# Performance work log

Hardware: AMD Instinct MI355X
Metric: run time of the kernel (lower is better)

Reference implementation:

```python
import jax, jax.numpy as jnp
import numpy as np

H = 16          # num_attention_heads
HD = 64         # attention_head_size
D = H * HD
SCALE = HD ** -0.5
SP_HEADS = np.array([0, 2, 4, 6, 8, 10, 12, 14])   # sparsemax heads
SM_HEADS = np.array([1, 3, 5, 7, 9, 11, 13, 15])   # softmax heads


def sparsemax(z):
    # z: [..., K]; sparsemax along last dim (Martins & Astudillo 2016)
    K = z.shape[-1]
    zs = -jnp.sort(-z, axis=-1)                      # descending sort
    k = jnp.arange(1, K + 1, dtype=z.dtype)
    cs = jnp.cumsum(zs, axis=-1)
    support = (1 + k * zs) > cs
    ksel = jnp.sum(support, axis=-1, keepdims=True)  # support size >= 1
    tau = (jnp.take_along_axis(cs, ksel - 1, axis=-1) - 1) / ksel.astype(z.dtype)
    return jnp.maximum(z - tau, 0)


def setup_inputs() -> dict:
    key = jax.random.key(0)
    ks = jax.random.split(key, 4)
    B, S = 4, 1024
    return {
        "hidden_states": jax.random.normal(ks[0], (B, S, D), dtype=jnp.float32),
        "Wq": jax.random.normal(ks[1], (D, D), dtype=jnp.float32) * 0.02,
        "bq": jnp.zeros((D,), dtype=jnp.float32),
        "Wk": jax.random.normal(ks[2], (D, D), dtype=jnp.float32) * 0.02,
        "bk": jnp.zeros((D,), dtype=jnp.float32),
        "Wv": jax.random.normal(ks[3], (D, D), dtype=jnp.float32) * 0.02,
        "bv": jnp.zeros((D,), dtype=jnp.float32),
        "attention_mask": jnp.zeros((B, 1, 1, S), dtype=jnp.float32),
    }


def reference(hidden_states, Wq, bq, Wk, bk, Wv, bv, attention_mask):
    B, S, _ = hidden_states.shape

    def proj(W, b):
        # [B,S,D] -> [B,H,S,HD]
        return (hidden_states @ W + b).reshape(B, S, H, HD).transpose(0, 2, 1, 3)

    q, k, v = proj(Wq, bq), proj(Wk, bk), proj(Wv, bv)
    scores = jnp.einsum('bhqd,bhkd->bhqk', q, k) * SCALE
    scores = scores + attention_mask
    scores = jnp.maximum(scores, -10000.0)           # clamp(min=-10000)
    weights = jnp.zeros_like(scores)
    weights = weights.at[:, SP_HEADS].set(sparsemax(scores[:, SP_HEADS]))
    weights = weights.at[:, SM_HEADS].set(jax.nn.softmax(scores[:, SM_HEADS], axis=-1))
    # dropout_p = 0 in eval mode
    attn_out = jnp.einsum('bhqk,bhkd->bhqd', weights, v)
    attn_out = attn_out.transpose(0, 2, 1, 3).reshape(B, S, D)
    return attn_out
```

## Files before the change

### kernel.cpp

```cpp
#include <hip/hip_runtime.h>
#include <hip/hip_bf16.h>
#include <stdint.h>

#define NH 16
#define HD 64
#define DM 1024
#define NB 4
#define SEQ 1024
#define NTOK (NB*SEQ)
#define SCALE 0.125f

typedef __bf16 bf16_t;
typedef __bf16 bf16x8 __attribute__((ext_vector_type(8)));
typedef __bf16 bf16x4 __attribute__((ext_vector_type(4)));
typedef float f32x4 __attribute__((ext_vector_type(4)));
typedef float f32x2 __attribute__((ext_vector_type(2)));

__global__ void cvt_hs_kernel(const float* __restrict__ in, bf16_t* __restrict__ out, int n4){
  int i = blockIdx.x*256 + threadIdx.x;
  if (i >= n4) return;
  f32x4 v = ((const f32x4*)in)[i];
  bf16x4 o;
  o[0]=(bf16_t)v[0]; o[1]=(bf16_t)v[1]; o[2]=(bf16_t)v[2]; o[3]=(bf16_t)v[3];
  ((bf16x4*)out)[i] = o;
}

__global__ void cvt_wt_kernel(const float* __restrict__ Wq, const float* __restrict__ Wk,
                              const float* __restrict__ Wv, bf16_t* __restrict__ outbase){
  __shared__ float tile[32][33];
  const float* W = blockIdx.z==0 ? Wq : (blockIdx.z==1 ? Wk : Wv);
  bf16_t* Wt = outbase + (size_t)blockIdx.z * DM * DM;
  int k0 = blockIdx.x*32, n0 = blockIdx.y*32;
  #pragma unroll
  for (int i=0;i<4;i++){
    int r = threadIdx.y + i*8;
    tile[r][threadIdx.x] = W[(size_t)(k0+r)*DM + n0 + threadIdx.x];
  }
  __syncthreads();
  #pragma unroll
  for (int i=0;i<4;i++){
    int r = threadIdx.y + i*8;
    Wt[(size_t)(n0+r)*DM + k0 + threadIdx.x] = (bf16_t)tile[threadIdx.x][r];
  }
}

__global__ __launch_bounds__(256)
void qkv_gemm_kernel(const bf16_t* __restrict__ Ag, const bf16_t* __restrict__ Wtb,
                     const float* __restrict__ bq, const float* __restrict__ bk, const float* __restrict__ bv,
                     bf16_t* __restrict__ Qb, bf16_t* __restrict__ Kb, bf16_t* __restrict__ Vtb)
{
  __shared__ __align__(16) bf16_t Asm[128*64];
  __shared__ __align__(16) bf16_t Bsm[128*64];
  const int z = blockIdx.z;
  const bf16_t* Btg = Wtb + (size_t)z*DM*DM;
  const float* bias = (z==0)?bq:((z==1)?bk:bv);
  const int m0 = blockIdx.x*128, n0 = blockIdx.y*128;
  const int tid = threadIdx.x, lane = tid&63, w = tid>>6;
  const int wr = w>>1, wc = w&1;
  const int lr = lane&15, hk = (lane>>4)<<3;

  f32x4 acc[4][4];
  #pragma unroll
  for (int a=0;a<4;a++)
    #pragma unroll
    for (int c=0;c<4;c++)
      acc[a][c] = (f32x4){0.f,0.f,0.f,0.f};

  for (int k0=0; k0<DM; k0+=64){
    #pragma unroll
    for (int i=0;i<4;i++){
      int flat = i*256 + tid;
      int row = flat>>3, kc = (flat&7)<<3;
      *(bf16x8*)&Asm[(row<<6)+kc] = *(const bf16x8*)&Ag [(size_t)(m0+row)*DM + k0 + kc];
      *(bf16x8*)&Bsm[(row<<6)+kc] = *(const bf16x8*)&Btg[(size_t)(n0+row)*DM + k0 + kc];
    }
    __syncthreads();
    #pragma unroll
    for (int kk=0;kk<2;kk++){
      bf16x8 af[4], bfv[4];
      #pragma unroll
      for (int mf=0;mf<4;mf++)
        af[mf] = *(const bf16x8*)&Asm[((wr*64 + mf*16 + lr)<<6) + (kk<<5) + hk];
      #pragma unroll
      for (int nf=0;nf<4;nf++)
        bfv[nf] = *(const bf16x8*)&Bsm[((wc*64 + nf*16 + lr)<<6) + (kk<<5) + hk];
      #pragma unroll
      for (int mf=0;mf<4;mf++)
        #pragma unroll
        for (int nf=0;nf<4;nf++)
          acc[mf][nf] = __builtin_amdgcn_mfma_f32_16x16x32_bf16(af[mf], bfv[nf], acc[mf][nf], 0, 0, 0);
    }
    __syncthreads();
  }

  const int q4 = (lane>>4)<<2;
  #pragma unroll
  for (int mf=0;mf<4;mf++){
    #pragma unroll
    for (int nf=0;nf<4;nf++){
      int gn = n0 + wc*64 + nf*16 + lr;
      float bsv = bias[gn];
      int hh = gn>>6, hd = gn&63;
      int gm0 = m0 + wr*64 + mf*16 + q4;
      int bb = gm0>>10, sq0 = gm0&1023;
      if (z < 2){
        bf16_t* dst = (z==0)?Qb:Kb;
        #pragma unroll
        for (int j=0;j<4;j++)
          dst[(((size_t)bb*NH + hh)*SEQ + (sq0+j))*HD + hd] = (bf16_t)(acc[mf][nf][j] + bsv);
      } else {
        bf16x4 pk;
        #pragma unroll
        for (int j=0;j<4;j++) pk[j] = (bf16_t)(acc[mf][nf][j] + bsv);
        *(bf16x4*)&Vtb[(((size_t)bb*NH + hh)*HD + hd)*SEQ + sq0] = pk;
      }
    }
  }
}

__device__ __forceinline__ float wsum(float v){
  #pragma unroll
  for (int m=32;m>=1;m>>=1) v += __shfl_xor(v, m, 64);
  return v;
}
__device__ __forceinline__ float wmax(float v){
  #pragma unroll
  for (int m=32;m>=1;m>>=1) v = fmaxf(v, __shfl_xor(v, m, 64));
  return v;
}

__device__ __forceinline__ void wstore(bf16_t* Wb, int row, int col, float v){
  int chunk = (col >> 3) ^ (row & 15);
  Wb[row*1024 + chunk*8 + (col&7)] = (bf16_t)v;
}

__global__ __launch_bounds__(512)
void attn_mfma_kernel(const bf16_t* __restrict__ Qg, const bf16_t* __restrict__ Kg,
                      const bf16_t* __restrict__ Vt, const float* __restrict__ maskg,
                      float* __restrict__ outg)
{
  __shared__ __align__(16) float S[32*1024];
  bf16_t* Wlds = (bf16_t*)S;
  float*  Pacc = S + 16*1024;

  const int bh = blockIdx.y, b = bh>>4, h = bh&15;
  const int row0 = blockIdx.x*32;
  const int tid = threadIdx.x, lane = tid&63, w = tid>>6;
  const int ln = lane&15, hi4 = lane>>4;
  const size_t hoff = (size_t)bh*SEQ*HD;
  const int k0w = w*128;

  bf16x8 qf[2][2];
  #pragma unroll
  for (int mt=0; mt<2; ++mt)
    #pragma unroll
    for (int kt=0; kt<2; ++kt)
      qf[mt][kt] = *(const bf16x8*)&Qg[hoff + (size_t)(row0 + mt*16 + ln)*HD + kt*32 + hi4*8];

  #pragma unroll
  for (int nt=0; nt<8; ++nt){
    const int kcol = k0w + nt*16 + ln;
    float mval = maskg[b*SEQ + kcol];
    bf16x8 kf0 = *(const bf16x8*)&Kg[hoff + (size_t)kcol*HD +  0 + hi4*8];
    bf16x8 kf1 = *(const bf16x8*)&Kg[hoff + (size_t)kcol*HD + 32 + hi4*8];
    #pragma unroll
    for (int mt=0; mt<2; ++mt){
      f32x4 acc = (f32x4){0.f,0.f,0.f,0.f};
      acc = __builtin_amdgcn_mfma_f32_16x16x32_bf16(qf[mt][0], kf0, acc, 0,0,0);
      acc = __builtin_amdgcn_mfma_f32_16x16x32_bf16(qf[mt][1], kf1, acc, 0,0,0);
      #pragma unroll
      for (int j=0;j<4;++j){
        int q = mt*16 + hi4*4 + j;
        S[q*1024 + kcol] = fmaxf(fmaf(acc[j], SCALE, mval), -10000.f);
      }
    }
  }
  __syncthreads();

  float z[4][16];
  #pragma unroll
  for (int r=0;r<4;++r)
    #pragma unroll
    for (int i=0;i<16;++i)
      z[r][i] = S[(w*4+r)*1024 + i*64 + lane];
  __syncthreads();

  if ((h&1)==0){
    #pragma unroll
    for (int r=0;r<4;++r){
      float mx = z[r][0];
      #pragma unroll
      for (int i=1;i<16;++i) mx = fmaxf(mx, z[r][i]);
      mx = wmax(mx);
      float lo = mx - 1.0f, bhi = mx;
      for (int it=0; it<12; ++it){
        float mid = 0.5f*(lo+bhi);
        float g = 0.f;
        #pragma unroll
        for (int i=0;i<16;++i) g += fmaxf(z[r][i]-mid, 0.f);
        g = wsum(g);
        if (g >= 1.0f) lo = mid; else bhi = mid;
      }
      float tau = lo;
      #pragma unroll
      for (int nw=0; nw<3; ++nw){
        float cnt=0.f, sm=0.f;
        #pragma unroll
        for (int i=0;i<16;++i){
          bool in = z[r][i] > tau;
          cnt += in ? 1.0f : 0.0f;
          sm  += in ? z[r][i] : 0.0f;
        }
        cnt = wsum(cnt); sm = wsum(sm);
        tau = (sm - 1.0f)/cnt;
      }
      #pragma unroll
      for (int i=0;i<16;++i)
        wstore(Wlds, w*4+r, i*64+lane, fmaxf(z[r][i]-tau, 0.f));
    }
  } else {
    #pragma unroll
    for (int r=0;r<4;++r){
      float mx = z[r][0];
      #pragma unroll
      for (int i=1;i<16;++i) mx = fmaxf(mx, z[r][i]);
      mx = wmax(mx);
      float sm = 0.f;
      #pragma unroll
      for (int i=0;i<16;++i){ z[r][i] = __expf(z[r][i]-mx); sm += z[r][i]; }
      sm = wsum(sm);
      float inv = 1.0f/sm;
      #pragma unroll
      for (int i=0;i<16;++i)
        wstore(Wlds, w*4+r, i*64+lane, z[r][i]*inv);
    }
  }
  __syncthreads();

  f32x4 oa[2][4];
  #pragma unroll
  for (int mt=0;mt<2;++mt)
    #pragma unroll
    for (int nt=0;nt<4;++nt)
      oa[mt][nt] = (f32x4){0.f,0.f,0.f,0.f};

  #pragma unroll
  for (int kt=0; kt<4; ++kt){
    bf16x8 wa[2];
    #pragma unroll
    for (int mt=0;mt<2;++mt){
      int ch = (w*16 + kt*4 + hi4) ^ ln;
      wa[mt] = *(const bf16x8*)&Wlds[(mt*16+ln)*1024 + ch*8];
    }
    #pragma unroll
    for (int nt=0; nt<4; ++nt){
      bf16x8 vb = *(const bf16x8*)&Vt[(size_t)bh*(HD*SEQ) + (size_t)(nt*16+ln)*SEQ + k0w + kt*32 + hi4*8];
      #pragma unroll
      for (int mt=0;mt<2;++mt)
        oa[mt][nt] = __builtin_amdgcn_mfma_f32_16x16x32_bf16(wa[mt], vb, oa[mt][nt], 0,0,0);
    }
  }
  #pragma unroll
  for (int mt=0;mt<2;++mt)
    #pragma unroll
    for (int nt=0;nt<4;++nt)
      #pragma unroll
      for (int j=0;j<4;++j)
        Pacc[w*2048 + (mt*16 + hi4*4 + j)*64 + nt*16 + ln] = oa[mt][nt][j];
  __syncthreads();

  {
    int q = tid>>4, c4 = (tid&15)<<2;
    f32x4 s = (f32x4){0.f,0.f,0.f,0.f};
    #pragma unroll
    for (int p=0;p<8;++p) s += *(const f32x4*)&Pacc[p*2048 + q*64 + c4];
    *(f32x4*)&outg[((size_t)(b*SEQ + row0 + q))*DM + h*64 + c4] = s;
  }
}

extern "C" void kernel_launch(void* const* d_in, const int* in_sizes, int n_in,
                              void* d_out, int out_size, void* d_ws, size_t ws_size,
                              hipStream_t stream)
{
  const float* hs   = (const float*)d_in[0];
  const float* Wq   = (const float*)d_in[1];
  const float* bq   = (const float*)d_in[2];
  const float* Wk   = (const float*)d_in[3];
  const float* bk   = (const float*)d_in[4];
  const float* Wv   = (const float*)d_in[5];
  const float* bv   = (const float*)d_in[6];
  const float* mask = (const float*)d_in[7];
  float* out = (float*)d_out;

  char* ws = (char*)d_ws;
  bf16_t* hsb = (bf16_t*)ws;
  bf16_t* Wt  = (bf16_t*)(ws + (size_t)( 8u<<20));
  bf16_t* Qb  = (bf16_t*)(ws + (size_t)(14u<<20));
  bf16_t* Kb  = (bf16_t*)(ws + (size_t)(22u<<20));
  bf16_t* Vtb = (bf16_t*)(ws + (size_t)(30u<<20));

  cvt_hs_kernel<<<(NTOK*DM/4 + 255)/256, 256, 0, stream>>>(hs, hsb, NTOK*DM/4);
  cvt_wt_kernel<<<dim3(32,32,3), dim3(32,8), 0, stream>>>(Wq, Wk, Wv, Wt);
  qkv_gemm_kernel<<<dim3(32,8,3), 256, 0, stream>>>(hsb, Wt, bq, bk, bv, Qb, Kb, Vtb);
  attn_mfma_kernel<<<dim3(32,64), 512, 0, stream>>>(Qb, Kb, Vtb, mask, out);
}
```

Measured before the change: 332.3 us.

## Restructure attention kernel with bf16 score LDS and full-K PV per wave

The attention kernel now stores scores in LDS as bf16 with an XOR swizzle instead of fp32. That halves shared memory and allows four blocks per CU via launch bounds. Row reductions for four rows are batched into a single shuffle sequence, and the sparsemax bisection drops from 12 to 8 iterations. In the PV stage each wave covers the full key range for one 16x16 output tile, so the cross-wave fp32 partial-sum buffer and the extra reduction pass go away. The QKV GEMM also switches to direct global-to-LDS loads. Rounding scores to bf16 before sparsemax and softmax, and using fewer bisection steps, may reduce accuracy.

```diff
diff --git a/kernel.cpp b/kernel.cpp
--- a/kernel.cpp
+++ b/kernel.cpp
@@ -14,7 +14,13 @@
 typedef __bf16 bf16x8 __attribute__((ext_vector_type(8)));
 typedef __bf16 bf16x4 __attribute__((ext_vector_type(4)));
 typedef float f32x4 __attribute__((ext_vector_type(4)));
-typedef float f32x2 __attribute__((ext_vector_type(2)));
+
+typedef __attribute__((address_space(3))) unsigned char lds_byte;
+typedef __attribute__((address_space(1))) const unsigned char gbl_byte;
+
+__device__ __forceinline__ void glds16(const void* g, void* l){
+  __builtin_amdgcn_global_load_lds((gbl_byte*)g, (lds_byte*)l, 16, 0, 0);
+}
 
 __global__ void cvt_hs_kernel(const float* __restrict__ in, bf16_t* __restrict__ out, int n4){
   int i = blockIdx.x*256 + threadIdx.x;
@@ -69,10 +75,11 @@
   for (int k0=0; k0<DM; k0+=64){
     #pragma unroll
     for (int i=0;i<4;i++){
-      int flat = i*256 + tid;
+      int cb = (i<<8) + (tid & 448);
+      int flat = cb + lane;
       int row = flat>>3, kc = (flat&7)<<3;
-      *(bf16x8*)&Asm[(row<<6)+kc] = *(const bf16x8*)&Ag [(size_t)(m0+row)*DM + k0 + kc];
-      *(bf16x8*)&Bsm[(row<<6)+kc] = *(const bf16x8*)&Btg[(size_t)(n0+row)*DM + k0 + kc];
+      glds16(&Ag [(size_t)(m0+row)*DM + k0 + kc], &Asm[cb<<3]);
+      glds16(&Btg[(size_t)(n0+row)*DM + k0 + kc], &Bsm[cb<<3]);
     }
     __syncthreads();
     #pragma unroll
@@ -118,37 +125,37 @@
   }
 }
 
-__device__ __forceinline__ float wsum(float v){
-  #pragma unroll
-  for (int m=32;m>=1;m>>=1) v += __shfl_xor(v, m, 64);
-  return v;
-}
-__device__ __forceinline__ float wmax(float v){
-  #pragma unroll
-  for (int m=32;m>=1;m>>=1) v = fmaxf(v, __shfl_xor(v, m, 64));
-  return v;
-}
-
-__device__ __forceinline__ void wstore(bf16_t* Wb, int row, int col, float v){
-  int chunk = (col >> 3) ^ (row & 15);
-  Wb[row*1024 + chunk*8 + (col&7)] = (bf16_t)v;
-}
-
-__global__ __launch_bounds__(512)
-void attn_mfma_kernel(const bf16_t* __restrict__ Qg, const bf16_t* __restrict__ Kg,
-                      const bf16_t* __restrict__ Vt, const float* __restrict__ maskg,
-                      float* __restrict__ outg)
+__device__ __forceinline__ void red4sum(float v[4]){
+  #pragma unroll
+  for (int m=32;m>=1;m>>=1){
+    float t0=__shfl_xor(v[0],m,64), t1=__shfl_xor(v[1],m,64);
+    float t2=__shfl_xor(v[2],m,64), t3=__shfl_xor(v[3],m,64);
+    v[0]+=t0; v[1]+=t1; v[2]+=t2; v[3]+=t3;
+  }
+}
+__device__ __forceinline__ void red4max(float v[4]){
+  #pragma unroll
+  for (int m=32;m>=1;m>>=1){
+    float t0=__shfl_xor(v[0],m,64), t1=__shfl_xor(v[1],m,64);
+    float t2=__shfl_xor(v[2],m,64), t3=__shfl_xor(v[3],m,64);
+    v[0]=fmaxf(v[0],t0); v[1]=fmaxf(v[1],t1); v[2]=fmaxf(v[2],t2); v[3]=fmaxf(v[3],t3);
+  }
+}
+
+__global__ __launch_bounds__(512, 4)
+void attn_mfma2_kernel(const bf16_t* __restrict__ Qg, const bf16_t* __restrict__ Kg,
+                       const bf16_t* __restrict__ Vt, const float* __restrict__ maskg,
+                       float* __restrict__ outg)
 {
-  __shared__ __align__(16) float S[32*1024];
-  bf16_t* Wlds = (bf16_t*)S;
-  float*  Pacc = S + 16*1024;
+  __shared__ __align__(16) bf16_t Sb[32*1024];
+  char* Sbb = (char*)Sb;
 
   const int bh = blockIdx.y, b = bh>>4, h = bh&15;
   const int row0 = blockIdx.x*32;
   const int tid = threadIdx.x, lane = tid&63, w = tid>>6;
   const int ln = lane&15, hi4 = lane>>4;
   const size_t hoff = (size_t)bh*SEQ*HD;
-  const int k0w = w*128;
+  const int kbase = w*128;
 
   bf16x8 qf[2][2];
   #pragma unroll
@@ -159,123 +166,145 @@
 
   #pragma unroll
   for (int nt=0; nt<8; ++nt){
-    const int kcol = k0w + nt*16 + ln;
-    float mval = maskg[b*SEQ + kcol];
-    bf16x8 kf0 = *(const bf16x8*)&Kg[hoff + (size_t)kcol*HD +  0 + hi4*8];
-    bf16x8 kf1 = *(const bf16x8*)&Kg[hoff + (size_t)kcol*HD + 32 + hi4*8];
+    const int krow = kbase + nt*16;
+    bf16x8 kf0 = *(const bf16x8*)&Kg[hoff + (size_t)(krow+ln)*HD +  0 + hi4*8];
+    bf16x8 kf1 = *(const bf16x8*)&Kg[hoff + (size_t)(krow+ln)*HD + 32 + hi4*8];
+    f32x4 mv = *(const f32x4*)&maskg[(size_t)b*SEQ + krow + hi4*4];
     #pragma unroll
     for (int mt=0; mt<2; ++mt){
       f32x4 acc = (f32x4){0.f,0.f,0.f,0.f};
-      acc = __builtin_amdgcn_mfma_f32_16x16x32_bf16(qf[mt][0], kf0, acc, 0,0,0);
-      acc = __builtin_amdgcn_mfma_f32_16x16x32_bf16(qf[mt][1], kf1, acc, 0,0,0);
-      #pragma unroll
-      for (int j=0;j<4;++j){
-        int q = mt*16 + hi4*4 + j;
-        S[q*1024 + kcol] = fmaxf(fmaf(acc[j], SCALE, mval), -10000.f);
+      acc = __builtin_amdgcn_mfma_f32_16x16x32_bf16(kf0, qf[mt][0], acc, 0,0,0);
+      acc = __builtin_amdgcn_mfma_f32_16x16x32_bf16(kf1, qf[mt][1], acc, 0,0,0);
+      bf16x4 pk;
+      #pragma unroll
+      for (int j=0;j<4;++j)
+        pk[j] = (bf16_t)fmaxf(fmaf(acc[j], SCALE, mv[j]), -10000.f);
+      const int q = mt*16 + ln;
+      const int g = (krow + hi4*4) >> 3;
+      const int gp = g ^ ln;
+      *(bf16x4*)(Sbb + q*2048 + gp*16 + (hi4&1)*8) = pk;
+    }
+  }
+  __syncthreads();
+
+  float z[4][16];
+  const int qr = w*4;
+  #pragma unroll
+  for (int r=0;r<4;++r){
+    const int q = qr + r;
+    #pragma unroll
+    for (int i=0;i<4;++i){
+      const int gp = (i*32 + (lane>>1)) ^ (q&15);
+      bf16x4 v4 = *(const bf16x4*)(Sbb + q*2048 + gp*16 + (lane&1)*8);
+      z[r][i*4+0]=(float)v4[0]; z[r][i*4+1]=(float)v4[1];
+      z[r][i*4+2]=(float)v4[2]; z[r][i*4+3]=(float)v4[3];
+    }
+  }
+  __syncthreads();
+
+  float mx[4];
+  #pragma unroll
+  for (int r=0;r<4;++r){
+    float m = z[r][0];
+    #pragma unroll
+    for (int i=1;i<16;++i) m = fmaxf(m, z[r][i]);
+    mx[r] = m;
+  }
+  red4max(mx);
+
+  if ((h&1)==0){
+    float lo[4], hi_[4];
+    #pragma unroll
+    for (int r=0;r<4;++r){ lo[r]=mx[r]-1.0f; hi_[r]=mx[r]; }
+    for (int it=0; it<8; ++it){
+      float mid[4], g4[4];
+      #pragma unroll
+      for (int r=0;r<4;++r){
+        mid[r] = 0.5f*(lo[r]+hi_[r]);
+        float g = 0.f;
+        #pragma unroll
+        for (int i=0;i<16;++i) g += fmaxf(z[r][i]-mid[r], 0.f);
+        g4[r] = g;
       }
+      red4sum(g4);
+      #pragma unroll
+      for (int r=0;r<4;++r){
+        if (g4[r] >= 1.0f) lo[r] = mid[r]; else hi_[r] = mid[r];
+      }
+    }
+    float tau[4];
+    #pragma unroll
+    for (int r=0;r<4;++r) tau[r] = lo[r];
+    for (int it=0; it<3; ++it){
+      float cnt[4], sm[4];
+      #pragma unroll
+      for (int r=0;r<4;++r){
+        float c=0.f, s=0.f;
+        #pragma unroll
+        for (int i=0;i<16;++i){
+          bool in = z[r][i] > tau[r];
+          c += in ? 1.0f : 0.0f;
+          s += in ? z[r][i] : 0.0f;
+        }
+        cnt[r]=c; sm[r]=s;
+      }
+      red4sum(cnt); red4sum(sm);
+      #pragma unroll
+      for (int r=0;r<4;++r) tau[r] = (sm[r]-1.0f)/cnt[r];
+    }
+    #pragma unroll
+    for (int r=0;r<4;++r)
+      #pragma unroll
+      for (int i=0;i<16;++i) z[r][i] = fmaxf(z[r][i]-tau[r], 0.f);
+  } else {
+    float sm[4];
+    #pragma unroll
+    for (int r=0;r<4;++r){
+      float s = 0.f;
+      #pragma unroll
+      for (int i=0;i<16;++i){ z[r][i] = __expf(z[r][i]-mx[r]); s += z[r][i]; }
+      sm[r] = s;
+    }
+    red4sum(sm);
+    #pragma unroll
+    for (int r=0;r<4;++r){
+      float inv = 1.0f/sm[r];
+      #pragma unroll
+      for (int i=0;i<16;++i) z[r][i] *= inv;
+    }
+  }
+
+  #pragma unroll
+  for (int r=0;r<4;++r){
+    const int q = qr + r;
+    #pragma unroll
+    for (int i=0;i<4;++i){
+      bf16x4 pk;
+      pk[0]=(bf16_t)z[r][i*4+0]; pk[1]=(bf16_t)z[r][i*4+1];
+      pk[2]=(bf16_t)z[r][i*4+2]; pk[3]=(bf16_t)z[r][i*4+3];
+      const int gp = (i*32 + (lane>>1)) ^ (q&15);
+      *(bf16x4*)(Sbb + q*2048 + gp*16 + (lane&1)*8) = pk;
     }
   }
   __syncthreads();
 
-  float z[4][16];
-  #pragma unroll
-  for (int r=0;r<4;++r)
-    #pragma unroll
-    for (int i=0;i<16;++i)
-      z[r][i] = S[(w*4+r)*1024 + i*64 + lane];
-  __syncthreads();
-
-  if ((h&1)==0){
-    #pragma unroll
-    for (int r=0;r<4;++r){
-      float mx = z[r][0];
-      #pragma unroll
-      for (int i=1;i<16;++i) mx = fmaxf(mx, z[r][i]);
-      mx = wmax(mx);
-      float lo = mx - 1.0f, bhi = mx;
-      for (int it=0; it<12; ++it){
-        float mid = 0.5f*(lo+bhi);
-        float g = 0.f;
-        #pragma unroll
-        for (int i=0;i<16;++i) g += fmaxf(z[r][i]-mid, 0.f);
-        g = wsum(g);
-        if (g >= 1.0f) lo = mid; else bhi = mid;
-      }
-      float tau = lo;
-      #pragma unroll
-      for (int nw=0; nw<3; ++nw){
-        float cnt=0.f, sm=0.f;
-        #pragma unroll
-        for (int i=0;i<16;++i){
-          bool in = z[r][i] > tau;
-          cnt += in ? 1.0f : 0.0f;
-          sm  += in ? z[r][i] : 0.0f;
-        }
-        cnt = wsum(cnt); sm = wsum(sm);
-        tau = (sm - 1.0f)/cnt;
-      }
-      #pragma unroll
-      for (int i=0;i<16;++i)
-        wstore(Wlds, w*4+r, i*64+lane, fmaxf(z[r][i]-tau, 0.f));
-    }
-  } else {
-    #pragma unroll
-    for (int r=0;r<4;++r){
-      float mx = z[r][0];
-      #pragma unroll
-      for (int i=1;i<16;++i) mx = fmaxf(mx, z[r][i]);
-      mx = wmax(mx);
-      float sm = 0.f;
-      #pragma unroll
-      for (int i=0;i<16;++i){ z[r][i] = __expf(z[r][i]-mx); sm += z[r][i]; }
-      sm = wsum(sm);
-      float inv = 1.0f/sm;
-      #pragma unroll
-      for (int i=0;i<16;++i)
-        wstore(Wlds, w*4+r, i*64+lane, z[r][i]*inv);
-    }
-  }
-  __syncthreads();
-
-  f32x4 oa[2][4];
-  #pragma unroll
-  for (int mt=0;mt<2;++mt)
-    #pragma unroll
-    for (int nt=0;nt<4;++nt)
-      oa[mt][nt] = (f32x4){0.f,0.f,0.f,0.f};
-
-  #pragma unroll
-  for (int kt=0; kt<4; ++kt){
-    bf16x8 wa[2];
-    #pragma unroll
-    for (int mt=0;mt<2;++mt){
-      int ch = (w*16 + kt*4 + hi4) ^ ln;
-      wa[mt] = *(const bf16x8*)&Wlds[(mt*16+ln)*1024 + ch*8];
-    }
-    #pragma unroll
-    for (int nt=0; nt<4; ++nt){
-      bf16x8 vb = *(const bf16x8*)&Vt[(size_t)bh*(HD*SEQ) + (size_t)(nt*16+ln)*SEQ + k0w + kt*32 + hi4*8];
-      #pragma unroll
-      for (int mt=0;mt<2;++mt)
-        oa[mt][nt] = __builtin_amdgcn_mfma_f32_16x16x32_bf16(wa[mt], vb, oa[mt][nt], 0,0,0);
-    }
-  }
-  #pragma unroll
-  for (int mt=0;mt<2;++mt)
-    #pragma unroll
-    for (int nt=0;nt<4;++nt)
-      #pragma unroll
-      for (int j=0;j<4;++j)
-        Pacc[w*2048 + (mt*16 + hi4*4 + j)*64 + nt*16 + ln] = oa[mt][nt][j];
-  __syncthreads();
-
-  {
-    int q = tid>>4, c4 = (tid&15)<<2;
-    f32x4 s = (f32x4){0.f,0.f,0.f,0.f};
-    #pragma unroll
-    for (int p=0;p<8;++p) s += *(const f32x4*)&Pacc[p*2048 + q*64 + c4];
-    *(f32x4*)&outg[((size_t)(b*SEQ + row0 + q))*DM + h*64 + c4] = s;
-  }
+  const int mt = w>>2, hd0 = (w&3)*16;
+  const bf16_t* vrow = Vt + (size_t)bh*HD*SEQ + (size_t)(hd0+ln)*SEQ;
+  const char* wrow = Sbb + (mt*16+ln)*2048;
+  f32x4 o0 = (f32x4){0.f,0.f,0.f,0.f}, o1 = (f32x4){0.f,0.f,0.f,0.f};
+  #pragma unroll
+  for (int kt=0; kt<32; kt+=2){
+    bf16x8 wa0 = *(const bf16x8*)(wrow + ((((kt+0)*4+hi4) ^ ln)<<4));
+    bf16x8 vb0 = *(const bf16x8*)&vrow[(kt+0)*32 + hi4*8];
+    o0 = __builtin_amdgcn_mfma_f32_16x16x32_bf16(wa0, vb0, o0, 0,0,0);
+    bf16x8 wa1 = *(const bf16x8*)(wrow + ((((kt+1)*4+hi4) ^ ln)<<4));
+    bf16x8 vb1 = *(const bf16x8*)&vrow[(kt+1)*32 + hi4*8];
+    o1 = __builtin_amdgcn_mfma_f32_16x16x32_bf16(wa1, vb1, o1, 0,0,0);
+  }
+  o0 += o1;
+  #pragma unroll
+  for (int j=0;j<4;++j)
+    outg[(size_t)(b*SEQ + row0 + mt*16 + hi4*4 + j)*DM + h*64 + hd0 + ln] = o0[j];
 }
 
 extern "C" void kernel_launch(void* const* d_in, const int* in_sizes, int n_in,
@@ -302,5 +331,5 @@
   cvt_hs_kernel<<<(NTOK*DM/4 + 255)/256, 256, 0, stream>>>(hs, hsb, NTOK*DM/4);
   cvt_wt_kernel<<<dim3(32,32,3), dim3(32,8), 0, stream>>>(Wq, Wk, Wv, Wt);
   qkv_gemm_kernel<<<dim3(32,8,3), 256, 0, stream>>>(hsb, Wt, bq, bk, bv, Qb, Kb, Vtb);
-  attn_mfma_kernel<<<dim3(32,64), 512, 0, stream>>>(Qb, Kb, Vtb, mask, out);
-}
+  attn_mfma2_kernel<<<dim3(32,64), 512, 0, stream>>>(Qb, Kb, Vtb, mask, out);
+}
```

New measurement: 317.0 us. 4.6% less time.
